# Kernel optimization log

Measured on AMD Instinct MI355X. Metric: run time of the kernel, lower is better.

Reference implementation:

```python
import jax, jax.numpy as jnp
import numpy as np

EPS = 1e-6
H = 16; D_NOPE = 128; D_ROPE = 64; D_V = 128; D_QK = D_NOPE + D_ROPE
Q_RANK = 1536; KV_RANK = 512; HID = 2048


def rmsnorm(x, w):
    var = jnp.mean(jnp.square(x.astype(jnp.float32)), axis=-1, keepdims=True)
    return (x * jax.lax.rsqrt(var + EPS)).astype(x.dtype) * w


def rotate_half(x):
    x1, x2 = jnp.split(x, 2, axis=-1)
    return jnp.concatenate([-x2, x1], axis=-1)


def interleave(x):
    # deepseek interleaved rope: pairs (0,1),(2,3).. -> [evens | odds]
    b, h, s, d = x.shape
    return x.reshape(b, h, s, d // 2, 2).transpose(0, 1, 2, 4, 3).reshape(b, h, s, d)


def setup_inputs() -> dict:
    key = jax.random.key(0)
    ks = jax.random.split(key, 8)
    B, S = 2, 2048
    sc = lambda n: 1.0 / np.sqrt(n)
    inp = {
        'hidden_states': jax.random.normal(ks[0], (B, S, HID), jnp.float32),
        'w_qa': jax.random.normal(ks[1], (HID, Q_RANK), jnp.float32) * sc(HID),
        'g_qa': jnp.ones((Q_RANK,), jnp.float32),
        'w_qb': jax.random.normal(ks[2], (Q_RANK, H * D_QK), jnp.float32) * sc(Q_RANK),
        'w_kva': jax.random.normal(ks[3], (HID, KV_RANK + D_ROPE), jnp.float32) * sc(HID),
        'g_kva': jnp.ones((KV_RANK,), jnp.float32),
        'w_kvb': jax.random.normal(ks[4], (KV_RANK, H * (D_NOPE + D_V)), jnp.float32) * sc(KV_RANK),
        'w_o': jax.random.normal(ks[5], (H * D_V, HID), jnp.float32) * sc(H * D_V),
    }
    pos = jnp.arange(S, dtype=jnp.float32)
    inv = 1.0 / (10000.0 ** (jnp.arange(0, D_ROPE, 2, dtype=jnp.float32) / D_ROPE))
    emb = jnp.concatenate([pos[:, None] * inv[None, :]] * 2, axis=-1)  # [S, 64]
    inp['cos'] = jnp.broadcast_to(jnp.cos(emb)[None], (B, S, D_ROPE))
    inp['sin'] = jnp.broadcast_to(jnp.sin(emb)[None], (B, S, D_ROPE))
    return inp


def reference(hidden_states, w_qa, g_qa, w_qb, w_kva, g_kva, w_kvb, w_o, cos, sin):
    B, S, _ = hidden_states.shape
    scaling = D_QK ** -0.5
    # low-rank Q: q_b_proj(q_a_layernorm(q_a_proj(h)))
    q = rmsnorm(hidden_states @ w_qa, g_qa) @ w_qb
    q = q.reshape(B, S, H, D_QK).transpose(0, 2, 1, 3)          # [B,H,S,192]
    q_pass, q_rot = q[..., :D_NOPE], q[..., D_NOPE:]
    # compressed KV latent + shared rope key
    ckv = hidden_states @ w_kva                                  # [B,S,576]
    k_pass, k_rot = ckv[..., :KV_RANK], ckv[..., KV_RANK:]
    kv = rmsnorm(k_pass, g_kva) @ w_kvb                          # [B,S,H*256]
    kv = kv.reshape(B, S, H, D_NOPE + D_V).transpose(0, 2, 1, 3)
    k_nope, v = kv[..., :D_NOPE], kv[..., D_NOPE:]
    k_rot = k_rot.reshape(B, 1, S, D_ROPE)
    c = cos[:, None, :, :]; sn = sin[:, None, :, :]
    q_rot = interleave(q_rot); k_rot = interleave(k_rot)
    q_rot = q_rot * c + rotate_half(q_rot) * sn
    k_rot = k_rot * c + rotate_half(k_rot) * sn
    k_rot = jnp.broadcast_to(k_rot, (B, H, S, D_ROPE))
    qf = jnp.concatenate([q_pass, q_rot], axis=-1)               # [B,H,S,192]
    kf = jnp.concatenate([k_nope, k_rot], axis=-1)               # [B,H,S,192]
    scores = jnp.einsum('bhqd,bhkd->bhqk', qf, kf) * scaling
    mask = jnp.triu(jnp.full((S, S), jnp.finfo(jnp.float32).min, jnp.float32), 1)
    probs = jax.nn.softmax(scores.astype(jnp.float32) + mask, axis=-1).astype(qf.dtype)
    out = jnp.einsum('bhqk,bhkd->bhqd', probs, v)                # [B,H,S,128]
    out = out.transpose(0, 2, 1, 3).reshape(B, S, H * D_V)
    return out @ w_o
```

## Files before the change

### kernel.cpp

```cpp
#include <hip/hip_runtime.h>

#define DI __device__ __forceinline__

typedef __attribute__((ext_vector_type(8))) unsigned short u16x8;
typedef __attribute__((ext_vector_type(8))) __bf16 bf16x8;
typedef __attribute__((ext_vector_type(4))) float f32x4;

constexpr int B_ = 2, S_ = 2048, H_ = 16, HID_ = 2048;
constexpr int QR = 1536, KVR = 512, DQK = 192;
constexpr int BS = B_ * S_;
constexpr float SCALE = 0.07216878364870323f;

DI unsigned short f2bf(float x){
  unsigned u = __builtin_bit_cast(unsigned, x);
  u = (u + 0x7FFFu + ((u >> 16) & 1u)) >> 16;
  return (unsigned short)u;
}
DI float bf2f(unsigned short h){
  return __builtin_bit_cast(float, ((unsigned)h) << 16);
}
DI f32x4 mfma16(u16x8 a, u16x8 b, f32x4 c){
  return __builtin_amdgcn_mfma_f32_16x16x32_bf16(
      __builtin_bit_cast(bf16x8, a), __builtin_bit_cast(bf16x8, b), c, 0, 0, 0);
}
DI void async16(const void* g, void* l){
  __builtin_amdgcn_global_load_lds(
      (__attribute__((address_space(1))) void*)(g),
      (__attribute__((address_space(3))) void*)(l), 16, 0, 0);
}

__global__ __launch_bounds__(256) void cvt_f32_bf16(const float* __restrict__ in,
                                                    unsigned short* __restrict__ out, int n8){
  const int i = blockIdx.x * 256 + threadIdx.x;
  if (i >= n8) return;
  const float4* pp = (const float4*)in + (long)i * 2;
  float4 a = pp[0], b = pp[1];
  u16x8 r;
  r[0]=f2bf(a.x); r[1]=f2bf(a.y); r[2]=f2bf(a.z); r[3]=f2bf(a.w);
  r[4]=f2bf(b.x); r[5]=f2bf(b.y); r[6]=f2bf(b.z); r[7]=f2bf(b.w);
  *(u16x8*)(out + (long)i * 8) = r;
}

__global__ __launch_bounds__(256) void wtrans(const float* __restrict__ W,
                                              unsigned short* __restrict__ Wt,
                                              int K, int N, int Np){
  __shared__ float t[32][33];
  const int n0 = blockIdx.x * 32, k0 = blockIdx.y * 32;
  const int tid = threadIdx.x;
  const int c = tid & 31, r0 = tid >> 5;
  #pragma unroll
  for (int i = 0; i < 4; ++i){
    const int r = r0 + i * 8;
    float v = 0.f;
    if (n0 + c < N) v = W[(long)(k0 + r) * N + n0 + c];
    t[r][c] = v;
  }
  __syncthreads();
  #pragma unroll
  for (int i = 0; i < 4; ++i){
    const int r = r0 + i * 8;
    Wt[(long)(n0 + r) * K + k0 + c] = f2bf(t[c][r]);
  }
}

template<int COLS>
__global__ __launch_bounds__(256) void rmsnorm_k(const float* __restrict__ X, int ldx,
                                                 const float* __restrict__ g,
                                                 unsigned short* __restrict__ Y, int ldy){
  constexpr int PT = COLS / 256;
  const int row = blockIdx.x, tid = threadIdx.x;
  const float* xr = X + (long)row * ldx;
  float v[PT];
  float ss = 0.f;
  #pragma unroll
  for (int i = 0; i < PT; ++i){ v[i] = xr[tid + i * 256]; ss += v[i] * v[i]; }
  #pragma unroll
  for (int off = 32; off >= 1; off >>= 1) ss += __shfl_xor(ss, off);
  __shared__ float red[4];
  if ((tid & 63) == 0) red[tid >> 6] = ss;
  __syncthreads();
  const float tot = red[0] + red[1] + red[2] + red[3];
  const float rs = rsqrtf(tot / (float)COLS + 1e-6f);
  #pragma unroll
  for (int i = 0; i < PT; ++i)
    Y[(long)row * ldy + tid + i * 256] = f2bf(v[i] * rs * g[tid + i * 256]);
}

template<bool OUT_BF16>
__global__ __launch_bounds__(256) void gemm_bt(const unsigned short* __restrict__ A,
                                               const unsigned short* __restrict__ Bt,
                                               void* __restrict__ Cv, int N, int K){
  __shared__ unsigned short lA[128 * 64];
  __shared__ unsigned short lB[128 * 64];
  const int tid = threadIdx.x;
  const int w = tid >> 6, lane = tid & 63, lr = lane & 15, lg = lane >> 4;
  const int wm = w >> 1, wn = w & 1;
  const long m0 = (long)blockIdx.y * 128, n0 = (long)blockIdx.x * 128;
  f32x4 acc[4][4] = {};
  const unsigned short* Ab = A + m0 * K;
  const unsigned short* Bb = Bt + n0 * K;
  for (int k0 = 0; k0 < K; k0 += 64){
    #pragma unroll
    for (int s2 = 0; s2 < 4; ++s2){
      const int c = s2 * 256 + tid;
      async16(Ab + (long)(c >> 3) * K + k0 + (c & 7) * 8, &lA[(s2 * 256 + w * 64) * 8]);
      async16(Bb + (long)(c >> 3) * K + k0 + (c & 7) * 8, &lB[(s2 * 256 + w * 64) * 8]);
    }
    __syncthreads();
    u16x8 a[2][4], b[2][4];
    #pragma unroll
    for (int kk = 0; kk < 2; ++kk){
      #pragma unroll
      for (int m = 0; m < 4; ++m)
        a[kk][m] = *(const u16x8*)&lA[(wm * 64 + m * 16 + lr) * 64 + kk * 32 + lg * 8];
      #pragma unroll
      for (int n = 0; n < 4; ++n)
        b[kk][n] = *(const u16x8*)&lB[(wn * 64 + n * 16 + lr) * 64 + kk * 32 + lg * 8];
    }
    #pragma unroll
    for (int kk = 0; kk < 2; ++kk)
      #pragma unroll
      for (int m = 0; m < 4; ++m)
        #pragma unroll
        for (int n = 0; n < 4; ++n)
          acc[m][n] = mfma16(a[kk][m], b[kk][n], acc[m][n]);
    __syncthreads();
  }
  #pragma unroll
  for (int m = 0; m < 4; ++m){
    const long row = m0 + wm * 64 + m * 16 + lg * 4;
    #pragma unroll
    for (int n = 0; n < 4; ++n){
      const long col = n0 + wn * 64 + n * 16 + lr;
      #pragma unroll
      for (int r = 0; r < 4; ++r){
        if (OUT_BF16) ((unsigned short*)Cv)[(row + r) * N + col] = f2bf(acc[m][n][r]);
        else          ((float*)Cv)[(row + r) * N + col] = acc[m][n][r];
      }
    }
  }
}

__global__ __launch_bounds__(256) void pack_q(const unsigned short* __restrict__ qm,
                                              const float* __restrict__ cosb,
                                              const float* __restrict__ sinb,
                                              unsigned short* __restrict__ qf){
  const int row = blockIdx.x, tid = threadIdx.x;
  const int b = row >> 11, s = row & 2047;
  const unsigned short* qr = qm + (long)row * 3072;
  const float* cr = cosb + (long)row * 64;
  const float* sr = sinb + (long)row * 64;
  #pragma unroll
  for (int it = 0; it < 12; ++it){
    const int o = it * 256 + tid;
    const int h = o / 192, d = o % 192;
    float val;
    if (d < 128) val = bf2f(qr[h * 192 + d]);
    else {
      const int i = d - 128, ii = i & 31;
      const float e  = bf2f(qr[h * 192 + 128 + 2 * ii]);
      const float od = bf2f(qr[h * 192 + 128 + 2 * ii + 1]);
      const float c = cr[ii], sn = sr[ii];
      val = (i < 32) ? (e * c - od * sn) : (od * c + e * sn);
    }
    qf[((long)(b * 16 + h) * S_ + s) * DQK + d] = f2bf(val * SCALE);
  }
}

__global__ __launch_bounds__(256) void pack_k(const unsigned short* __restrict__ kvm,
                                              const float* __restrict__ ckv,
                                              const float* __restrict__ cosb,
                                              const float* __restrict__ sinb,
                                              unsigned short* __restrict__ kf){
  const int row = blockIdx.x, tid = threadIdx.x;
  const int b = row >> 11, s = row & 2047;
  const unsigned short* kr = kvm + (long)row * 4096;
  const float* cv = ckv + (long)row * 640 + 512;
  const float* cr = cosb + (long)row * 64;
  const float* sr = sinb + (long)row * 64;
  #pragma unroll
  for (int it = 0; it < 12; ++it){
    const int o = it * 256 + tid;
    const int h = o / 192, d = o % 192;
    unsigned short val;
    if (d < 128) val = kr[h * 256 + d];
    else {
      const int i = d - 128, ii = i & 31;
      const float e = cv[2 * ii], od = cv[2 * ii + 1];
      const float c = cr[ii], sn = sr[ii];
      val = f2bf((i < 32) ? (e * c - od * sn) : (od * c + e * sn));
    }
    kf[((long)(b * 16 + h) * S_ + s) * DQK + d] = val;
  }
}

__global__ __launch_bounds__(256) void pack_v(const unsigned short* __restrict__ kvm,
                                              unsigned short* __restrict__ vt){
  const int bh = blockIdx.x, s0 = blockIdx.y * 64;
  const int b = bh >> 4, h = bh & 15;
  __shared__ unsigned short t[64][130];
  #pragma unroll
  for (int it = 0; it < 32; ++it){
    const int idx = it * 256 + threadIdx.x;
    const int sl = idx >> 7, d = idx & 127;
    t[sl][d] = kvm[(long)(b * S_ + s0 + sl) * 4096 + h * 256 + 128 + d];
  }
  __syncthreads();
  #pragma unroll
  for (int it = 0; it < 32; ++it){
    const int idx = it * 256 + threadIdx.x;
    const int dr = idx >> 6, sc = idx & 63;
    vt[(long)(bh * 128 + dr) * S_ + s0 + sc] = t[sc][dr];
  }
}

__global__ __launch_bounds__(256) void mla_attn(const unsigned short* __restrict__ qf,
                                                const unsigned short* __restrict__ kf,
                                                const unsigned short* __restrict__ vt,
                                                unsigned short* __restrict__ ao){
  __shared__ unsigned short k_lds[64 * 192];
  __shared__ unsigned short v_lds[128 * 64];
  __shared__ unsigned short p_lds[4][32][72];
  const int bid = blockIdx.x;
  const int u = bid >> 5;
  const int qt = (u < 8) ? u : 23 - u;
  const int bh = bid & 31;
  const int b = bh >> 4, h = bh & 15;
  const int tid = threadIdx.x;
  const int w = tid >> 6, lane = tid & 63, lr = lane & 15, lg = lane >> 4;
  const int q0 = qt * 128 + w * 32;
  const unsigned short* qb = qf + (long)bh * S_ * DQK;
  const unsigned short* kb = kf + (long)bh * S_ * DQK;
  const unsigned short* vb = vt + (long)bh * 128 * S_;
  u16x8 aq[2][6];
  #pragma unroll
  for (int mi = 0; mi < 2; ++mi)
    #pragma unroll
    for (int kk = 0; kk < 6; ++kk)
      aq[mi][kk] = *(const u16x8*)&qb[(long)(q0 + mi * 16 + lr) * DQK + kk * 32 + lg * 8];
  f32x4 oacc[2][8] = {};
  f32x4 lacc[2] = {};
  float mrun[2][4];
  #pragma unroll
  for (int mi = 0; mi < 2; ++mi)
    #pragma unroll
    for (int r = 0; r < 4; ++r) mrun[mi][r] = -1e30f;
  u16x8 onesv;
  #pragma unroll
  for (int i = 0; i < 8; ++i) onesv[i] = 0x3F80;
  const int ktiles = (qt + 1) * 2;
  const int myktiles = ((q0 + 31) >> 6) + 1;
  for (int kt = 0; kt < ktiles; ++kt){
    #pragma unroll
    for (int s2 = 0; s2 < 6; ++s2){
      const int c = s2 * 256 + tid;
      const int row = c / 24, col = c - row * 24;
      async16(kb + (long)(kt * 64 + row) * DQK + ((col ^ (row & 7)) << 3),
              &k_lds[(s2 * 256 + w * 64) * 8]);
    }
    #pragma unroll
    for (int s2 = 0; s2 < 4; ++s2){
      const int c = s2 * 256 + tid;
      const int row = c >> 3, col = c & 7;
      async16(vb + (long)row * S_ + kt * 64 + ((col ^ (row & 7)) << 3),
              &v_lds[(s2 * 256 + w * 64) * 8]);
    }
    __syncthreads();
    if (kt < myktiles){
      f32x4 sacc[2][4] = {};
      #pragma unroll
      for (int ni = 0; ni < 4; ++ni){
        const int rowk = ni * 16 + lr;
        #pragma unroll
        for (int kk = 0; kk < 6; ++kk){
          const int col16 = kk * 4 + lg;
          const u16x8 bk = *(const u16x8*)&k_lds[rowk * 192 + ((col16 ^ (rowk & 7)) << 3)];
          sacc[0][ni] = mfma16(aq[0][kk], bk, sacc[0][ni]);
          sacc[1][ni] = mfma16(aq[1][kk], bk, sacc[1][ni]);
        }
      }
      const int kbase = kt * 64;
      if (kbase + 63 > q0){
        #pragma unroll
        for (int mi = 0; mi < 2; ++mi)
          #pragma unroll
          for (int r = 0; r < 4; ++r){
            const int qrow = q0 + mi * 16 + lg * 4 + r;
            #pragma unroll
            for (int ni = 0; ni < 4; ++ni)
              if (kbase + ni * 16 + lr > qrow) sacc[mi][ni][r] = -1e30f;
          }
      }
      #pragma unroll
      for (int mi = 0; mi < 2; ++mi)
        #pragma unroll
        for (int r = 0; r < 4; ++r){
          float tm = fmaxf(fmaxf(sacc[mi][0][r], sacc[mi][1][r]),
                           fmaxf(sacc[mi][2][r], sacc[mi][3][r]));
          tm = fmaxf(tm, __shfl_xor(tm, 1));
          tm = fmaxf(tm, __shfl_xor(tm, 2));
          tm = fmaxf(tm, __shfl_xor(tm, 4));
          tm = fmaxf(tm, __shfl_xor(tm, 8));
          if (tm > mrun[mi][r]){
            const float sc = __expf(mrun[mi][r] - tm);
            mrun[mi][r] = tm;
            lacc[mi][r] *= sc;
            #pragma unroll
            for (int d = 0; d < 8; ++d) oacc[mi][d][r] *= sc;
          }
          const float m_ = mrun[mi][r];
          const int qq = mi * 16 + lg * 4 + r;
          #pragma unroll
          for (int ni = 0; ni < 4; ++ni)
            p_lds[w][qq][ni * 16 + lr] = f2bf(__expf(sacc[mi][ni][r] - m_));
        }
      u16x8 pa[2][2];
      #pragma unroll
      for (int mi = 0; mi < 2; ++mi)
        #pragma unroll
        for (int kk2 = 0; kk2 < 2; ++kk2)
          pa[mi][kk2] = *(const u16x8*)&p_lds[w][mi * 16 + lr][kk2 * 32 + lg * 8];
      #pragma unroll
      for (int mi = 0; mi < 2; ++mi)
        #pragma unroll
        for (int kk2 = 0; kk2 < 2; ++kk2)
          lacc[mi] = mfma16(pa[mi][kk2], onesv, lacc[mi]);
      #pragma unroll
      for (int d = 0; d < 8; ++d){
        const int rowv = d * 16 + lr;
        #pragma unroll
        for (int kk2 = 0; kk2 < 2; ++kk2){
          const int col16 = kk2 * 4 + lg;
          const u16x8 bv = *(const u16x8*)&v_lds[rowv * 64 + ((col16 ^ (rowv & 7)) << 3)];
          oacc[0][d] = mfma16(pa[0][kk2], bv, oacc[0][d]);
          oacc[1][d] = mfma16(pa[1][kk2], bv, oacc[1][d]);
        }
      }
    }
    __syncthreads();
  }
  #pragma unroll
  for (int mi = 0; mi < 2; ++mi)
    #pragma unroll
    for (int r = 0; r < 4; ++r){
      const long row = q0 + mi * 16 + lg * 4 + r;
      const float inv = 1.0f / lacc[mi][r];
      #pragma unroll
      for (int d = 0; d < 8; ++d)
        ao[(long)(b * S_ + row) * 2048 + h * 128 + d * 16 + lr] = f2bf(oacc[mi][d][r] * inv);
    }
}

extern "C" void kernel_launch(void* const* d_in, const int* in_sizes, int n_in,
                              void* d_out, int out_size, void* d_ws, size_t ws_size,
                              hipStream_t stream){
  const float* hid   = (const float*)d_in[0];
  const float* w_qa  = (const float*)d_in[1];
  const float* g_qa  = (const float*)d_in[2];
  const float* w_qb  = (const float*)d_in[3];
  const float* w_kva = (const float*)d_in[4];
  const float* g_kva = (const float*)d_in[5];
  const float* w_kvb = (const float*)d_in[6];
  const float* w_o   = (const float*)d_in[7];
  const float* cosb  = (const float*)d_in[8];
  const float* sinb  = (const float*)d_in[9];
  float* out = (float*)d_out;

  char* p = (char*)d_ws;
  auto alloc = [&](size_t bytes) -> void* {
    void* r = p;
    p += (bytes + 255) & ~(size_t)255;
    return r;
  };
  unsigned short* hb     = (unsigned short*)alloc((size_t)BS * HID_ * 2);
  unsigned short* wqa_t  = (unsigned short*)alloc((size_t)QR * HID_ * 2);
  unsigned short* wqb_t  = (unsigned short*)alloc((size_t)3072 * QR * 2);
  unsigned short* wkva_t = (unsigned short*)alloc((size_t)640 * HID_ * 2);
  unsigned short* wkvb_t = (unsigned short*)alloc((size_t)4096 * KVR * 2);
  unsigned short* wo_t   = (unsigned short*)alloc((size_t)2048 * 2048 * 2);
  float*          qa_f   = (float*)alloc((size_t)BS * QR * 4);
  unsigned short* qan    = (unsigned short*)alloc((size_t)BS * QR * 2);
  float*          ckv_f  = (float*)alloc((size_t)BS * 640 * 4);
  unsigned short* kvn    = (unsigned short*)alloc((size_t)BS * KVR * 2);
  unsigned short* qmat   = (unsigned short*)alloc((size_t)BS * 3072 * 2);
  unsigned short* kvmat  = (unsigned short*)alloc((size_t)BS * 4096 * 2);
  unsigned short* qfb    = (unsigned short*)alloc((size_t)32 * S_ * DQK * 2);
  unsigned short* kfb    = (unsigned short*)alloc((size_t)32 * S_ * DQK * 2);
  unsigned short* vtb    = (unsigned short*)alloc((size_t)32 * 128 * S_ * 2);
  unsigned short* aob    = (unsigned short*)alloc((size_t)BS * 2048 * 2);
  (void)ws_size; (void)in_sizes; (void)n_in; (void)out_size;

  cvt_f32_bf16<<<BS * HID_ / 8 / 256, 256, 0, stream>>>(hid, hb, BS * HID_ / 8);
  wtrans<<<dim3(1536 / 32, 2048 / 32), 256, 0, stream>>>(w_qa, wqa_t, 2048, 1536, 1536);
  wtrans<<<dim3(3072 / 32, 1536 / 32), 256, 0, stream>>>(w_qb, wqb_t, 1536, 3072, 3072);
  wtrans<<<dim3(640 / 32, 2048 / 32), 256, 0, stream>>>(w_kva, wkva_t, 2048, 576, 640);
  wtrans<<<dim3(4096 / 32, 512 / 32), 256, 0, stream>>>(w_kvb, wkvb_t, 512, 4096, 4096);
  wtrans<<<dim3(2048 / 32, 2048 / 32), 256, 0, stream>>>(w_o, wo_t, 2048, 2048, 2048);

  gemm_bt<false><<<dim3(1536 / 128, BS / 128), 256, 0, stream>>>(hb, wqa_t, qa_f, 1536, 2048);
  gemm_bt<false><<<dim3(640 / 128, BS / 128), 256, 0, stream>>>(hb, wkva_t, ckv_f, 640, 2048);
  rmsnorm_k<1536><<<BS, 256, 0, stream>>>(qa_f, 1536, g_qa, qan, 1536);
  rmsnorm_k<512><<<BS, 256, 0, stream>>>(ckv_f, 640, g_kva, kvn, 512);
  gemm_bt<true><<<dim3(3072 / 128, BS / 128), 256, 0, stream>>>(qan, wqb_t, qmat, 3072, 1536);
  gemm_bt<true><<<dim3(4096 / 128, BS / 128), 256, 0, stream>>>(kvn, wkvb_t, kvmat, 4096, 512);

  pack_q<<<BS, 256, 0, stream>>>(qmat, cosb, sinb, qfb);
  pack_k<<<BS, 256, 0, stream>>>(kvmat, ckv_f, cosb, sinb, kfb);
  pack_v<<<dim3(32, S_ / 64), 256, 0, stream>>>(kvmat, vtb);

  mla_attn<<<512, 256, 0, stream>>>(qfb, kfb, vtb, aob);

  gemm_bt<false><<<dim3(2048 / 128, BS / 128), 256, 0, stream>>>(aob, wo_t, out, 2048, 2048);
}
```

Measured before the change: 604.2 us.

## Fuse Q/KV pack into GEMM epilogues, use exp2 softmax and hardware bf16 convert

The Q up-projection GEMM now applies RoPE, scaling and the head-major scatter directly in its epilogue, and the KV up-projection writes k_nope straight into the packed K buffer. This removes the intermediate qmat buffer and the pack_q/pack_k passes. The Q scale folds in log2(e) so the attention softmax can use exp2, and the running-max rescale is deferred until the max grows by more than 8. f2bf now uses the hardware v_cvt_pk_bf16_f32 instruction. The trade-offs are scattered epilogue stores and a lazy rescale that lets unnormalized probabilities grow larger before rescaling.

```diff
diff --git a/kernel.cpp b/kernel.cpp
--- a/kernel.cpp
+++ b/kernel.cpp
@@ -10,11 +10,12 @@
 constexpr int QR = 1536, KVR = 512, DQK = 192;
 constexpr int BS = B_ * S_;
 constexpr float SCALE = 0.07216878364870323f;
+constexpr float QS = SCALE * 1.4426950408889634f;
 
 DI unsigned short f2bf(float x){
-  unsigned u = __builtin_bit_cast(unsigned, x);
-  u = (u + 0x7FFFu + ((u >> 16) & 1u)) >> 16;
-  return (unsigned short)u;
+  unsigned r;
+  asm("v_cvt_pk_bf16_f32 %0, %1, %2" : "=v"(r) : "v"(x), "v"(x));
+  return (unsigned short)r;
 }
 DI float bf2f(unsigned short h){
   return __builtin_bit_cast(float, ((unsigned)h) << 16);
@@ -86,10 +87,9 @@
     Y[(long)row * ldy + tid + i * 256] = f2bf(v[i] * rs * g[tid + i * 256]);
 }
 
-template<bool OUT_BF16>
 __global__ __launch_bounds__(256) void gemm_bt(const unsigned short* __restrict__ A,
                                                const unsigned short* __restrict__ Bt,
-                                               void* __restrict__ Cv, int N, int K){
+                                               float* __restrict__ C, int N, int K){
   __shared__ unsigned short lA[128 * 64];
   __shared__ unsigned short lB[128 * 64];
   const int tid = threadIdx.x;
@@ -133,64 +133,160 @@
     for (int n = 0; n < 4; ++n){
       const long col = n0 + wn * 64 + n * 16 + lr;
       #pragma unroll
+      for (int r = 0; r < 4; ++r)
+        C[(row + r) * N + col] = acc[m][n][r];
+    }
+  }
+}
+
+__global__ __launch_bounds__(256) void gemm_qpack(const unsigned short* __restrict__ A,
+                                                  const unsigned short* __restrict__ Bt,
+                                                  const float* __restrict__ cosb,
+                                                  const float* __restrict__ sinb,
+                                                  unsigned short* __restrict__ qf, int K){
+  const int N = 3072;
+  __shared__ unsigned short lA[128 * 64];
+  __shared__ unsigned short lB[128 * 64];
+  const int tid = threadIdx.x;
+  const int w = tid >> 6, lane = tid & 63, lr = lane & 15, lg = lane >> 4;
+  const int wm = w >> 1, wn = w & 1;
+  const long m0 = (long)blockIdx.y * 128, n0 = (long)blockIdx.x * 128;
+  f32x4 acc[4][4] = {};
+  const unsigned short* Ab = A + m0 * K;
+  const unsigned short* Bb = Bt + n0 * K;
+  for (int k0 = 0; k0 < K; k0 += 64){
+    #pragma unroll
+    for (int s2 = 0; s2 < 4; ++s2){
+      const int c = s2 * 256 + tid;
+      async16(Ab + (long)(c >> 3) * K + k0 + (c & 7) * 8, &lA[(s2 * 256 + w * 64) * 8]);
+      async16(Bb + (long)(c >> 3) * K + k0 + (c & 7) * 8, &lB[(s2 * 256 + w * 64) * 8]);
+    }
+    __syncthreads();
+    u16x8 a[2][4], b[2][4];
+    #pragma unroll
+    for (int kk = 0; kk < 2; ++kk){
+      #pragma unroll
+      for (int m = 0; m < 4; ++m)
+        a[kk][m] = *(const u16x8*)&lA[(wm * 64 + m * 16 + lr) * 64 + kk * 32 + lg * 8];
+      #pragma unroll
+      for (int n = 0; n < 4; ++n)
+        b[kk][n] = *(const u16x8*)&lB[(wn * 64 + n * 16 + lr) * 64 + kk * 32 + lg * 8];
+    }
+    #pragma unroll
+    for (int kk = 0; kk < 2; ++kk)
+      #pragma unroll
+      for (int m = 0; m < 4; ++m)
+        #pragma unroll
+        for (int n = 0; n < 4; ++n)
+          acc[m][n] = mfma16(a[kk][m], b[kk][n], acc[m][n]);
+    __syncthreads();
+  }
+  #pragma unroll
+  for (int m = 0; m < 4; ++m){
+    const int rowg = (int)m0 + wm * 64 + m * 16 + lg * 4;
+    #pragma unroll
+    for (int n = 0; n < 4; ++n){
+      const int col = (int)n0 + wn * 64 + n * 16 + lr;
+      const int h = (unsigned)col / 192u;
+      const int d = col - h * 192;
+      #pragma unroll
       for (int r = 0; r < 4; ++r){
-        if (OUT_BF16) ((unsigned short*)Cv)[(row + r) * N + col] = f2bf(acc[m][n][r]);
-        else          ((float*)Cv)[(row + r) * N + col] = acc[m][n][r];
+        const int rowi = rowg + r;
+        const float a = acc[m][n][r];
+        const float partner = __shfl_xor(a, 1);
+        float val; int dout;
+        if (d < 128){ val = a; dout = d; }
+        else {
+          const int ii = (d - 128) >> 1;
+          const float c  = cosb[(long)rowi * 64 + ii];
+          const float sn = sinb[(long)rowi * 64 + ii];
+          val  = (d & 1) ? (a * c + partner * sn) : (a * c - partner * sn);
+          dout = 128 + ((d & 1) << 5) + ii;
+        }
+        const int b = rowi >> 11, s = rowi & 2047;
+        qf[((long)(b * 16 + h) * S_ + s) * DQK + dout] = f2bf(val * QS);
       }
     }
   }
 }
 
-__global__ __launch_bounds__(256) void pack_q(const unsigned short* __restrict__ qm,
-                                              const float* __restrict__ cosb,
-                                              const float* __restrict__ sinb,
-                                              unsigned short* __restrict__ qf){
+__global__ __launch_bounds__(256) void gemm_kvpack(const unsigned short* __restrict__ A,
+                                                   const unsigned short* __restrict__ Bt,
+                                                   unsigned short* __restrict__ kf,
+                                                   unsigned short* __restrict__ kvm, int K){
+  const int N = 4096;
+  __shared__ unsigned short lA[128 * 64];
+  __shared__ unsigned short lB[128 * 64];
+  const int tid = threadIdx.x;
+  const int w = tid >> 6, lane = tid & 63, lr = lane & 15, lg = lane >> 4;
+  const int wm = w >> 1, wn = w & 1;
+  const long m0 = (long)blockIdx.y * 128, n0 = (long)blockIdx.x * 128;
+  f32x4 acc[4][4] = {};
+  const unsigned short* Ab = A + m0 * K;
+  const unsigned short* Bb = Bt + n0 * K;
+  for (int k0 = 0; k0 < K; k0 += 64){
+    #pragma unroll
+    for (int s2 = 0; s2 < 4; ++s2){
+      const int c = s2 * 256 + tid;
+      async16(Ab + (long)(c >> 3) * K + k0 + (c & 7) * 8, &lA[(s2 * 256 + w * 64) * 8]);
+      async16(Bb + (long)(c >> 3) * K + k0 + (c & 7) * 8, &lB[(s2 * 256 + w * 64) * 8]);
+    }
+    __syncthreads();
+    u16x8 a[2][4], b[2][4];
+    #pragma unroll
+    for (int kk = 0; kk < 2; ++kk){
+      #pragma unroll
+      for (int m = 0; m < 4; ++m)
+        a[kk][m] = *(const u16x8*)&lA[(wm * 64 + m * 16 + lr) * 64 + kk * 32 + lg * 8];
+      #pragma unroll
+      for (int n = 0; n < 4; ++n)
+        b[kk][n] = *(const u16x8*)&lB[(wn * 64 + n * 16 + lr) * 64 + kk * 32 + lg * 8];
+    }
+    #pragma unroll
+    for (int kk = 0; kk < 2; ++kk)
+      #pragma unroll
+      for (int m = 0; m < 4; ++m)
+        #pragma unroll
+        for (int n = 0; n < 4; ++n)
+          acc[m][n] = mfma16(a[kk][m], b[kk][n], acc[m][n]);
+    __syncthreads();
+  }
+  #pragma unroll
+  for (int m = 0; m < 4; ++m){
+    const int rowg = (int)m0 + wm * 64 + m * 16 + lg * 4;
+    #pragma unroll
+    for (int n = 0; n < 4; ++n){
+      const int col = (int)n0 + wn * 64 + n * 16 + lr;
+      const int h = col >> 8, d = col & 255;
+      #pragma unroll
+      for (int r = 0; r < 4; ++r){
+        const int rowi = rowg + r;
+        const unsigned short v = f2bf(acc[m][n][r]);
+        const int b = rowi >> 11, s = rowi & 2047;
+        if (d < 128) kf[((long)(b * 16 + h) * S_ + s) * DQK + d] = v;
+        else         kvm[(long)rowi * 4096 + col] = v;
+      }
+    }
+  }
+}
+
+__global__ __launch_bounds__(256) void pack_krot(const float* __restrict__ ckv,
+                                                 const float* __restrict__ cosb,
+                                                 const float* __restrict__ sinb,
+                                                 unsigned short* __restrict__ kf){
   const int row = blockIdx.x, tid = threadIdx.x;
   const int b = row >> 11, s = row & 2047;
-  const unsigned short* qr = qm + (long)row * 3072;
-  const float* cr = cosb + (long)row * 64;
-  const float* sr = sinb + (long)row * 64;
-  #pragma unroll
-  for (int it = 0; it < 12; ++it){
-    const int o = it * 256 + tid;
-    const int h = o / 192, d = o % 192;
-    float val;
-    if (d < 128) val = bf2f(qr[h * 192 + d]);
-    else {
-      const int i = d - 128, ii = i & 31;
-      const float e  = bf2f(qr[h * 192 + 128 + 2 * ii]);
-      const float od = bf2f(qr[h * 192 + 128 + 2 * ii + 1]);
-      const float c = cr[ii], sn = sr[ii];
-      val = (i < 32) ? (e * c - od * sn) : (od * c + e * sn);
-    }
-    qf[((long)(b * 16 + h) * S_ + s) * DQK + d] = f2bf(val * SCALE);
-  }
-}
-
-__global__ __launch_bounds__(256) void pack_k(const unsigned short* __restrict__ kvm,
-                                              const float* __restrict__ ckv,
-                                              const float* __restrict__ cosb,
-                                              const float* __restrict__ sinb,
-                                              unsigned short* __restrict__ kf){
-  const int row = blockIdx.x, tid = threadIdx.x;
-  const int b = row >> 11, s = row & 2047;
-  const unsigned short* kr = kvm + (long)row * 4096;
   const float* cv = ckv + (long)row * 640 + 512;
   const float* cr = cosb + (long)row * 64;
   const float* sr = sinb + (long)row * 64;
   #pragma unroll
-  for (int it = 0; it < 12; ++it){
-    const int o = it * 256 + tid;
-    const int h = o / 192, d = o % 192;
-    unsigned short val;
-    if (d < 128) val = kr[h * 256 + d];
-    else {
-      const int i = d - 128, ii = i & 31;
-      const float e = cv[2 * ii], od = cv[2 * ii + 1];
-      const float c = cr[ii], sn = sr[ii];
-      val = f2bf((i < 32) ? (e * c - od * sn) : (od * c + e * sn));
-    }
-    kf[((long)(b * 16 + h) * S_ + s) * DQK + d] = val;
+  for (int j = 0; j < 4; ++j){
+    const int o = j * 256 + tid;
+    const int h = o >> 6, i = o & 63, ii = i & 31;
+    const float e = cv[2 * ii], od = cv[2 * ii + 1];
+    const float c = cr[ii], sn = sr[ii];
+    const float val = (i < 32) ? (e * c - od * sn) : (od * c + e * sn);
+    kf[((long)(b * 16 + h) * S_ + s) * DQK + 128 + i] = f2bf(val);
   }
 }
 
@@ -301,8 +397,8 @@
           tm = fmaxf(tm, __shfl_xor(tm, 2));
           tm = fmaxf(tm, __shfl_xor(tm, 4));
           tm = fmaxf(tm, __shfl_xor(tm, 8));
-          if (tm > mrun[mi][r]){
-            const float sc = __expf(mrun[mi][r] - tm);
+          if (tm > mrun[mi][r] + 8.f){
+            const float sc = __builtin_exp2f(mrun[mi][r] - tm);
             mrun[mi][r] = tm;
             lacc[mi][r] *= sc;
             #pragma unroll
@@ -310,9 +406,10 @@
           }
           const float m_ = mrun[mi][r];
           const int qq = mi * 16 + lg * 4 + r;
-          #pragma unroll
-          for (int ni = 0; ni < 4; ++ni)
-            p_lds[w][qq][ni * 16 + lr] = f2bf(__expf(sacc[mi][ni][r] - m_));
+          p_lds[w][qq][lr]      = f2bf(__builtin_exp2f(sacc[mi][0][r] - m_));
+          p_lds[w][qq][16 + lr] = f2bf(__builtin_exp2f(sacc[mi][1][r] - m_));
+          p_lds[w][qq][32 + lr] = f2bf(__builtin_exp2f(sacc[mi][2][r] - m_));
+          p_lds[w][qq][48 + lr] = f2bf(__builtin_exp2f(sacc[mi][3][r] - m_));
         }
       u16x8 pa[2][2];
       #pragma unroll
@@ -382,7 +479,6 @@
   unsigned short* qan    = (unsigned short*)alloc((size_t)BS * QR * 2);
   float*          ckv_f  = (float*)alloc((size_t)BS * 640 * 4);
   unsigned short* kvn    = (unsigned short*)alloc((size_t)BS * KVR * 2);
-  unsigned short* qmat   = (unsigned short*)alloc((size_t)BS * 3072 * 2);
   unsigned short* kvmat  = (unsigned short*)alloc((size_t)BS * 4096 * 2);
   unsigned short* qfb    = (unsigned short*)alloc((size_t)32 * S_ * DQK * 2);
   unsigned short* kfb    = (unsigned short*)alloc((size_t)32 * S_ * DQK * 2);
@@ -397,18 +493,17 @@
   wtrans<<<dim3(4096 / 32, 512 / 32), 256, 0, stream>>>(w_kvb, wkvb_t, 512, 4096, 4096);
   wtrans<<<dim3(2048 / 32, 2048 / 32), 256, 0, stream>>>(w_o, wo_t, 2048, 2048, 2048);
 
-  gemm_bt<false><<<dim3(1536 / 128, BS / 128), 256, 0, stream>>>(hb, wqa_t, qa_f, 1536, 2048);
-  gemm_bt<false><<<dim3(640 / 128, BS / 128), 256, 0, stream>>>(hb, wkva_t, ckv_f, 640, 2048);
+  gemm_bt<<<dim3(1536 / 128, BS / 128), 256, 0, stream>>>(hb, wqa_t, qa_f, 1536, 2048);
+  gemm_bt<<<dim3(640 / 128, BS / 128), 256, 0, stream>>>(hb, wkva_t, ckv_f, 640, 2048);
   rmsnorm_k<1536><<<BS, 256, 0, stream>>>(qa_f, 1536, g_qa, qan, 1536);
   rmsnorm_k<512><<<BS, 256, 0, stream>>>(ckv_f, 640, g_kva, kvn, 512);
-  gemm_bt<true><<<dim3(3072 / 128, BS / 128), 256, 0, stream>>>(qan, wqb_t, qmat, 3072, 1536);
-  gemm_bt<true><<<dim3(4096 / 128, BS / 128), 256, 0, stream>>>(kvn, wkvb_t, kvmat, 4096, 512);
-
-  pack_q<<<BS, 256, 0, stream>>>(qmat, cosb, sinb, qfb);
-  pack_k<<<BS, 256, 0, stream>>>(kvmat, ckv_f, cosb, sinb, kfb);
+
+  gemm_qpack<<<dim3(3072 / 128, BS / 128), 256, 0, stream>>>(qan, wqb_t, cosb, sinb, qfb, 1536);
+  gemm_kvpack<<<dim3(4096 / 128, BS / 128), 256, 0, stream>>>(kvn, wkvb_t, kfb, kvmat, 512);
+  pack_krot<<<BS, 256, 0, stream>>>(ckv_f, cosb, sinb, kfb);
   pack_v<<<dim3(32, S_ / 64), 256, 0, stream>>>(kvmat, vtb);
 
   mla_attn<<<512, 256, 0, stream>>>(qfb, kfb, vtb, aob);
 
-  gemm_bt<false><<<dim3(2048 / 128, BS / 128), 256, 0, stream>>>(aob, wo_t, out, 2048, 2048);
-}
+  gemm_bt<<<dim3(2048 / 128, BS / 128), 256, 0, stream>>>(aob, wo_t, out, 2048, 2048);
+}
```

After: 609.2 us. Within noise of the previous version (+0.8%).
